# Performance work log

Hardware: AMD Instinct MI355X
Metric: run time of the kernel (lower is better)

The kernel has to match this reference:

```python
import jax, jax.numpy as jnp
import numpy as np

MAX_ITEMS = 100000
WEIGHT0 = 0.1
MOMENT = 0.9
INV_WARM_UP = 1.0 / 1000.0
INV_COOL_DOWN = 1.0 / 100000.0


def setup_inputs() -> dict:
    key = jax.random.key(0)
    k1, k2, k3 = jax.random.split(key, 3)
    activations = jax.random.normal(k1, (4096, 512), dtype=jnp.float32)
    history = jax.random.normal(k2, (MAX_ITEMS + 1, 512), dtype=jnp.float32)
    samples = jax.random.randint(k3, (4096,), 0, MAX_ITEMS + 1, dtype=jnp.int64)
    return {"activations": activations, "history": history,
            "samples": samples, "iterations": 5000}


def reference(activations, history, samples, iterations):
    # mask: ids strictly in (0, max_items); clamp indices into table range
    mask = jnp.logical_and(samples > 0, samples < MAX_ITEMS).astype(activations.dtype)
    ids = jnp.minimum(samples, MAX_ITEMS)

    old = history[ids]  # gather: (B, D)

    # mse objective: mean over last axis -> (B,)
    per_sample = jnp.mean(jnp.square(activations - old), axis=-1)

    it = jnp.asarray(iterations, dtype=activations.dtype)
    wr = INV_WARM_UP * it
    cr = INV_COOL_DOWN * it
    weight = WEIGHT0 * wr / (1.0 + wr) / (1.0 + cr)
    loss = jnp.mean(per_sample * mask) * weight

    # EMA history update: history[ids] -= (1 - moment) * (old - act) * mask
    diff = (old - activations) * mask[:, None]
    new_history = history.at[ids].add(-(1.0 - MOMENT) * diff)

    return activations, loss, new_history
```

## Files before the change

### kernel.cpp

```cpp
#include <hip/hip_runtime.h>

#define MAX_ITEMS 100000
constexpr int B = 4096;
constexpr int D = 512;
constexpr long long ACT_ELEMS  = (long long)B * D;
constexpr long long HIST_ELEMS = (long long)(MAX_ITEMS + 1) * D;

template <int KU>
__global__ void copy_act_kernel(const float* __restrict__ act,
                                const float* __restrict__ hist,
                                float* __restrict__ out) {
    constexpr long long NA4 = ACT_ELEMS / 4;
    const long long chunk = (long long)blockDim.x * KU;
    for (long long c = blockIdx.x; c * chunk < NA4; c += gridDim.x) {
        const long long g0 = c * chunk + threadIdx.x;
        float4 v[KU];
        #pragma unroll
        for (int k = 0; k < KU; ++k)
            v[k] = reinterpret_cast<const float4*>(act)[g0 + (long long)k * blockDim.x];
        #pragma unroll
        for (int k = 0; k < KU; ++k)
            reinterpret_cast<float4*>(out)[g0 + (long long)k * blockDim.x] = v[k];
    }
    if (blockIdx.x == 0 && threadIdx.x == 0) {
        float* outh = out + ACT_ELEMS + 1;
        outh[0] = hist[0];
        outh[1] = hist[1];
        outh[2] = hist[2];
        outh[HIST_ELEMS - 1] = hist[HIST_ELEMS - 1];
    }
}

template <int KU>
__global__ void copy_hist_kernel(const float* __restrict__ hist,
                                 float* __restrict__ out) {
    constexpr long long NG = (HIST_ELEMS - 3) / 4;
    float* __restrict__ outh = out + ACT_ELEMS + 1;
    const long long chunk = (long long)blockDim.x * KU;
    for (long long c = blockIdx.x; c * chunk < NG; c += gridDim.x) {
        const long long g0 = c * chunk + threadIdx.x;
        float4 v[KU];
        #pragma unroll
        for (int k = 0; k < KU; ++k) {
            const long long g = g0 + (long long)k * blockDim.x;
            if (g < NG) {
                const long long sb = 3 + 4 * g;
                v[k].x = hist[sb + 0];
                v[k].y = hist[sb + 1];
                v[k].z = hist[sb + 2];
                v[k].w = hist[sb + 3];
            }
        }
        #pragma unroll
        for (int k = 0; k < KU; ++k) {
            const long long g = g0 + (long long)k * blockDim.x;
            if (g < NG)
                *reinterpret_cast<float4*>(outh + 3 + 4 * g) = v[k];
        }
    }
}

__global__ void update_kernel(const float* __restrict__ act,
                              const float* __restrict__ hist,
                              const int* __restrict__ samples,
                              float* __restrict__ out,
                              float* __restrict__ partial) {
    const int s    = blockIdx.x;
    const int lane = threadIdx.x;

    const int id = samples[s];
    const bool active = (id > 0) && (id < MAX_ITEMS);

    float sumsq = 0.0f;
    if (active) {
        const float* __restrict__ arow = act  + (long long)s  * D;
        const float* __restrict__ orow = hist + (long long)id * D;
        float* __restrict__ newh = out + ACT_ELEMS + 1 + (long long)id * D;

        #pragma unroll
        for (int k = 0; k < 2; ++k) {
            const int e = (lane + k * 64) * 4;
            const float4 a = *reinterpret_cast<const float4*>(arow + e);
            const float4 o = *reinterpret_cast<const float4*>(orow + e);
            const float dx = a.x - o.x;
            const float dy = a.y - o.y;
            const float dz = a.z - o.z;
            const float dw = a.w - o.w;
            sumsq += dx * dx + dy * dy + dz * dz + dw * dw;
            atomicAdd(newh + e + 0, 0.1f * dx);
            atomicAdd(newh + e + 1, 0.1f * dy);
            atomicAdd(newh + e + 2, 0.1f * dz);
            atomicAdd(newh + e + 3, 0.1f * dw);
        }
    }
    #pragma unroll
    for (int off = 32; off; off >>= 1)
        sumsq += __shfl_down(sumsq, off);
    if (lane == 0) partial[s] = sumsq;
}

__global__ void loss_kernel(const float* __restrict__ partial,
                            const int* __restrict__ iters,
                            float* __restrict__ out) {
    __shared__ float sm[256];
    const int t = threadIdx.x;
    float s = 0.0f;
    for (int i = t; i < B; i += 256) s += partial[i];
    sm[t] = s;
    __syncthreads();
    #pragma unroll
    for (int w = 128; w; w >>= 1) {
        if (t < w) sm[t] += sm[t + w];
        __syncthreads();
    }
    if (t == 0) {
        const float it = (float)iters[0];
        const float wr = (float)(1.0 / 1000.0)   * it;
        const float cr = (float)(1.0 / 100000.0) * it;
        const float weight = 0.1f * wr / (1.0f + wr) / (1.0f + cr);
        out[ACT_ELEMS] = (sm[0] / (float)D / (float)B) * weight;
    }
}

extern "C" void kernel_launch(void* const* d_in, const int* in_sizes, int n_in,
                              void* d_out, int out_size, void* d_ws, size_t ws_size,
                              hipStream_t stream) {
    const float* act     = (const float*)d_in[0];
    const float* hist    = (const float*)d_in[1];
    const int*   samples = (const int*)d_in[2];
    const int*   iters   = (const int*)d_in[3];
    float* out     = (float*)d_out;
    float* partial = (float*)d_ws;

    copy_hist_kernel<8><<<2048, 256, 0, stream>>>(hist, out);
    copy_act_kernel<8><<<256, 256, 0, stream>>>(act, hist, out);
    update_kernel<<<B, 64, 0, stream>>>(act, hist, samples, out, partial);
    loss_kernel<<<1, 256, 0, stream>>>(partial, iters, out);
}
```

Baseline: 133.3 us.

## Use aligned float4 loads with lane shuffles for history copy; fuse activation copy into update

The history copy into the output (offset by ACT_ELEMS+1, so misaligned by one float) now reads aligned float4 vectors and builds each shifted output vector with wavefront shuffles, doing a scalar fetch only for the last lane of each wave. This replaces four scalar loads per output vector. The separate activation copy kernel is removed: each update block copies its own activation row, which saves one launch and lets the activation row be read once for both the copy and the difference. The cost is extra shuffle instructions in the copy loop and the boundary element writes moving into the history kernel.

```diff
diff --git a/kernel.cpp b/kernel.cpp
--- a/kernel.cpp
+++ b/kernel.cpp
@@ -7,56 +7,44 @@
 constexpr long long HIST_ELEMS = (long long)(MAX_ITEMS + 1) * D;
 
 template <int KU>
-__global__ void copy_act_kernel(const float* __restrict__ act,
-                                const float* __restrict__ hist,
-                                float* __restrict__ out) {
-    constexpr long long NA4 = ACT_ELEMS / 4;
-    const long long chunk = (long long)blockDim.x * KU;
-    for (long long c = blockIdx.x; c * chunk < NA4; c += gridDim.x) {
-        const long long g0 = c * chunk + threadIdx.x;
-        float4 v[KU];
-        #pragma unroll
-        for (int k = 0; k < KU; ++k)
-            v[k] = reinterpret_cast<const float4*>(act)[g0 + (long long)k * blockDim.x];
-        #pragma unroll
-        for (int k = 0; k < KU; ++k)
-            reinterpret_cast<float4*>(out)[g0 + (long long)k * blockDim.x] = v[k];
-    }
-    if (blockIdx.x == 0 && threadIdx.x == 0) {
-        float* outh = out + ACT_ELEMS + 1;
-        outh[0] = hist[0];
-        outh[1] = hist[1];
-        outh[2] = hist[2];
-        outh[HIST_ELEMS - 1] = hist[HIST_ELEMS - 1];
-    }
-}
-
-template <int KU>
 __global__ void copy_hist_kernel(const float* __restrict__ hist,
                                  float* __restrict__ out) {
     constexpr long long NG = (HIST_ELEMS - 3) / 4;
     float* __restrict__ outh = out + ACT_ELEMS + 1;
+    const float4* __restrict__ src = reinterpret_cast<const float4*>(hist);
+    const int lane = threadIdx.x & 63;
     const long long chunk = (long long)blockDim.x * KU;
+
     for (long long c = blockIdx.x; c * chunk < NG; c += gridDim.x) {
         const long long g0 = c * chunk + threadIdx.x;
         float4 v[KU];
         #pragma unroll
         for (int k = 0; k < KU; ++k) {
             const long long g = g0 + (long long)k * blockDim.x;
-            if (g < NG) {
-                const long long sb = 3 + 4 * g;
-                v[k].x = hist[sb + 0];
-                v[k].y = hist[sb + 1];
-                v[k].z = hist[sb + 2];
-                v[k].w = hist[sb + 3];
-            }
+            if (g <= NG) v[k] = src[g];
         }
         #pragma unroll
         for (int k = 0; k < KU; ++k) {
             const long long g = g0 + (long long)k * blockDim.x;
-            if (g < NG)
-                *reinterpret_cast<float4*>(outh + 3 + 4 * g) = v[k];
+            float nx = __shfl_down(v[k].x, 1);
+            float ny = __shfl_down(v[k].y, 1);
+            float nz = __shfl_down(v[k].z, 1);
+            if (g < NG) {
+                if (lane == 63) {
+                    nx = hist[4 * (g + 1) + 0];
+                    ny = hist[4 * (g + 1) + 1];
+                    nz = hist[4 * (g + 1) + 2];
+                }
+                *reinterpret_cast<float4*>(outh + 3 + 4 * g) =
+                    make_float4(v[k].w, nx, ny, nz);
+            }
         }
+    }
+    if (blockIdx.x == 0 && threadIdx.x == 0) {
+        outh[0] = hist[0];
+        outh[1] = hist[1];
+        outh[2] = hist[2];
+        outh[HIST_ELEMS - 1] = hist[HIST_ELEMS - 1];
     }
 }
 
@@ -68,25 +56,39 @@
     const int s    = blockIdx.x;
     const int lane = threadIdx.x;
 
+    const float4* __restrict__ arow = reinterpret_cast<const float4*>(act + (long long)s * D);
+    float4* __restrict__ aout = reinterpret_cast<float4*>(out + (long long)s * D);
+    const float4 a0 = arow[lane];
+    const float4 a1 = arow[lane + 64];
+    aout[lane]      = a0;
+    aout[lane + 64] = a1;
+
     const int id = samples[s];
     const bool active = (id > 0) && (id < MAX_ITEMS);
 
     float sumsq = 0.0f;
     if (active) {
-        const float* __restrict__ arow = act  + (long long)s  * D;
-        const float* __restrict__ orow = hist + (long long)id * D;
+        const float4* __restrict__ orow =
+            reinterpret_cast<const float4*>(hist + (long long)id * D);
         float* __restrict__ newh = out + ACT_ELEMS + 1 + (long long)id * D;
+        const float4 o0 = orow[lane];
+        const float4 o1 = orow[lane + 64];
 
-        #pragma unroll
-        for (int k = 0; k < 2; ++k) {
-            const int e = (lane + k * 64) * 4;
-            const float4 a = *reinterpret_cast<const float4*>(arow + e);
-            const float4 o = *reinterpret_cast<const float4*>(orow + e);
-            const float dx = a.x - o.x;
-            const float dy = a.y - o.y;
-            const float dz = a.z - o.z;
-            const float dw = a.w - o.w;
+        {
+            const float dx = a0.x - o0.x, dy = a0.y - o0.y;
+            const float dz = a0.z - o0.z, dw = a0.w - o0.w;
             sumsq += dx * dx + dy * dy + dz * dz + dw * dw;
+            const int e = lane * 4;
+            atomicAdd(newh + e + 0, 0.1f * dx);
+            atomicAdd(newh + e + 1, 0.1f * dy);
+            atomicAdd(newh + e + 2, 0.1f * dz);
+            atomicAdd(newh + e + 3, 0.1f * dw);
+        }
+        {
+            const float dx = a1.x - o1.x, dy = a1.y - o1.y;
+            const float dz = a1.z - o1.z, dw = a1.w - o1.w;
+            sumsq += dx * dx + dy * dy + dz * dz + dw * dw;
+            const int e = (lane + 64) * 4;
             atomicAdd(newh + e + 0, 0.1f * dx);
             atomicAdd(newh + e + 1, 0.1f * dy);
             atomicAdd(newh + e + 2, 0.1f * dz);
@@ -133,7 +135,6 @@
     float* partial = (float*)d_ws;
 
     copy_hist_kernel<8><<<2048, 256, 0, stream>>>(hist, out);
-    copy_act_kernel<8><<<256, 256, 0, stream>>>(act, hist, out);
     update_kernel<<<B, 64, 0, stream>>>(act, hist, samples, out, partial);
     loss_kernel<<<1, 256, 0, stream>>>(partial, iters, out);
 }
```

Result: no change. 134.9 us (+1.1%).
